# Optimization experiments

Measured on AMD Instinct MI355X. Metric: run time of the kernel, lower is better.

Reference implementation:

```python
import jax, jax.numpy as jnp
import numpy as np

SEG = 8  # conv1d groups


def _grouped_mix(y, W2, b2, seg):
    # y: [b, C_in, L]; W2: [C_out, C_in//seg]; grouped 1x1 conv1d
    b_, cin, L = y.shape
    cout = W2.shape[0]
    yg = y.reshape(b_, seg, cin // seg, L)
    Wg = W2.reshape(seg, cout // seg, cin // seg)
    z = jnp.einsum('bgcl,goc->bgol', yg, Wg).reshape(b_, cout, L)
    return z + b2[None, :, None]


def _mix_h(x, W1, b1, W2, b2):
    # x: [b,h,w,d]
    b_, H, Wd, D = x.shape
    y = jnp.einsum('bhwd,ed->bhwe', x, W1) + b1            # 1x1 conv2d -> [b,h,w,e]
    y = jnp.transpose(y, (0, 3, 1, 2)).reshape(b_, -1, Wd)  # 'b d h w -> b (d h) w'
    z = _grouped_mix(y, W2, b2, SEG)                        # [b, h*h, w]
    attn = jax.nn.softmax(
        z.reshape(b_, H, H, Wd).transpose(0, 3, 1, 2), axis=-1)  # [b,w,h1,h2]
    xr = jnp.transpose(x, (0, 2, 1, 3))                     # [b,w,h,d]
    out = jnp.einsum('bwij,bwjd->bwid', attn, xr)
    return jnp.transpose(out, (0, 2, 1, 3))                 # [b,h,w,d]


def _mix_w(x, W1, b1, W2, b2):
    # x: [b,h,w,d]
    b_, H, Wd, D = x.shape
    y = jnp.einsum('bhwd,ed->bhwe', x, W1) + b1             # [b,h,w,e]
    y = jnp.transpose(y, (0, 3, 2, 1)).reshape(b_, -1, H)   # 'b d w h -> b (d w) h'
    z = _grouped_mix(y, W2, b2, SEG)                        # [b, w*w, h]
    attn = jax.nn.softmax(
        z.reshape(b_, Wd, Wd, H).transpose(0, 3, 1, 2), axis=-1)  # [b,h,w1,w2]
    return jnp.einsum('bhij,bhjd->bhid', attn, x)           # [b,h,w,d]


def setup_inputs() -> dict:
    key = jax.random.key(0)
    ks = jax.random.split(key, 16)
    B, H, W, D, E = 64, 32, 32, 384, 2
    s = 0.05
    return {
        'x':   jax.random.normal(ks[0], (B, H, W, D), jnp.float32),
        'Wc':  jax.random.normal(ks[1], (D, D), jnp.float32) * s,
        'bc':  jnp.zeros((D,), jnp.float32),
        'Wo':  jax.random.normal(ks[2], (D, D), jnp.float32) * s,
        'bo':  jnp.zeros((D,), jnp.float32),
        'W1h': jax.random.normal(ks[3], (E, D), jnp.float32) * s,
        'b1h': jnp.zeros((E,), jnp.float32),
        'W2h': jax.random.normal(ks[4], (H * H, E * H // SEG), jnp.float32) * s,
        'b2h': jnp.zeros((H * H,), jnp.float32),
        'W1w': jax.random.normal(ks[5], (E, D), jnp.float32) * s,
        'b1w': jnp.zeros((E,), jnp.float32),
        'W2w': jax.random.normal(ks[6], (W * W, E * W // SEG), jnp.float32) * s,
        'b2w': jnp.zeros((W * W,), jnp.float32),
    }


def reference(x, Wc, bc, Wo, bo, W1h, b1h, W2h, b2h, W1w, b1w, W2w, b2w):
    Y_c = jnp.einsum('bhwd,od->bhwo', x, Wc) + bc
    Y_h = _mix_h(x, W1h, b1h, W2h, b2h)
    Y_w = _mix_w(x, W1w, b1w, W2w, b2w)
    Y = Y_h + Y_w + Y_c
    return jnp.einsum('bhwd,od->bhwo', Y, Wo) + bo
```

## Files before the change

### kernel.cpp

```cpp
#include <hip/hip_runtime.h>
#include <hip/hip_bf16.h>
#include <cstdint>
#include <cstddef>

typedef __bf16 bf16;
typedef __attribute__((ext_vector_type(8))) __bf16 bf16x8;
typedef __attribute__((ext_vector_type(4))) float floatx4;

#define NPIX 65536

__device__ inline void async_copy16(void* lds, const void* g) {
    __builtin_amdgcn_global_load_lds(
        (const __attribute__((address_space(1))) void*)g,
        (__attribute__((address_space(3))) void*)lds, 16, 0, 0);
}

__global__ void k_prep_w(const float* __restrict__ Wc, const float* __restrict__ bc,
                         const float* __restrict__ Wo, const float* __restrict__ bo,
                         bf16* __restrict__ Wfull, float* __restrict__ bco) {
    int blk = blockIdx.x;
    int t = threadIdx.x;
    if (blk < 384) {
        int o = blk;
        float acc = 0.f;
        for (int d = 0; d < 384; ++d)
            acc += Wo[o * 384 + d] * Wc[d * 384 + t];
        Wfull[(size_t)o * 768 + t]       = (bf16)Wo[o * 384 + t];
        Wfull[(size_t)o * 768 + 384 + t] = (bf16)acc;
    } else {
        int o = t;
        float acc = bo[o];
        for (int d = 0; d < 384; ++d)
            acc += Wo[o * 384 + d] * bc[d];
        bco[o] = acc;
    }
}

__global__ void k_proj(const float* __restrict__ xf, bf16* __restrict__ xb,
                       const float* __restrict__ W1h, const float* __restrict__ b1h,
                       const float* __restrict__ W1w, const float* __restrict__ b1w,
                       float* __restrict__ yh, float* __restrict__ yw) {
    int t  = threadIdx.x;
    int lg = t & 7;
    int pg = t >> 3;
    int p  = blockIdx.x * 32 + pg;
    int b = p >> 10, h = (p >> 5) & 31, w = p & 31;
    const float4* xp4 = (const float4*)(xf + (size_t)p * 384);
    float a0 = 0.f, a1 = 0.f, a2 = 0.f, a3 = 0.f;
#pragma unroll
    for (int j = 0; j < 6; ++j) {
        int c = j * 8 + lg;
        float4 xa = xp4[c * 2], xcv = xp4[c * 2 + 1];
        bf16x8 v;
        v[0] = (bf16)xa.x; v[1] = (bf16)xa.y; v[2] = (bf16)xa.z; v[3] = (bf16)xa.w;
        v[4] = (bf16)xcv.x; v[5] = (bf16)xcv.y; v[6] = (bf16)xcv.z; v[7] = (bf16)xcv.w;
        *(bf16x8*)(xb + ((size_t)(c >> 1) * NPIX + p) * 16 + (c & 1) * 8) = v;
        const float4* h0 = (const float4*)(W1h + c * 8);
        const float4* h1 = (const float4*)(W1h + 384 + c * 8);
        const float4* w0 = (const float4*)(W1w + c * 8);
        const float4* w1 = (const float4*)(W1w + 384 + c * 8);
        float4 h0a = h0[0], h0b = h0[1], h1a = h1[0], h1b = h1[1];
        float4 w0a = w0[0], w0b = w0[1], w1a = w1[0], w1b = w1[1];
        a0 += xa.x*h0a.x + xa.y*h0a.y + xa.z*h0a.z + xa.w*h0a.w
            + xcv.x*h0b.x + xcv.y*h0b.y + xcv.z*h0b.z + xcv.w*h0b.w;
        a1 += xa.x*h1a.x + xa.y*h1a.y + xa.z*h1a.z + xa.w*h1a.w
            + xcv.x*h1b.x + xcv.y*h1b.y + xcv.z*h1b.z + xcv.w*h1b.w;
        a2 += xa.x*w0a.x + xa.y*w0a.y + xa.z*w0a.z + xa.w*w0a.w
            + xcv.x*w0b.x + xcv.y*w0b.y + xcv.z*w0b.z + xcv.w*w0b.w;
        a3 += xa.x*w1a.x + xa.y*w1a.y + xa.z*w1a.z + xa.w*w1a.w
            + xcv.x*w1b.x + xcv.y*w1b.y + xcv.z*w1b.z + xcv.w*w1b.w;
    }
#pragma unroll
    for (int m = 1; m < 8; m <<= 1) {
        a0 += __shfl_xor(a0, m, 64);
        a1 += __shfl_xor(a1, m, 64);
        a2 += __shfl_xor(a2, m, 64);
        a3 += __shfl_xor(a3, m, 64);
    }
    if (lg == 0) {
        yh[((b * 2 + 0) * 32 + h) * 32 + w] = a0 + b1h[0];
        yh[((b * 2 + 1) * 32 + h) * 32 + w] = a1 + b1h[1];
        yw[((b * 2 + 0) * 32 + w) * 32 + h] = a2 + b1w[0];
        yw[((b * 2 + 1) * 32 + w) * 32 + h] = a3 + b1w[1];
    }
}

__global__ void k_attn(const float* __restrict__ yproj,
                       const float* __restrict__ W2, const float* __restrict__ b2,
                       bf16* __restrict__ attn) {
    int blk = blockIdx.x;
    int bi = blk >> 5, r1 = blk & 31;
    int g = r1 >> 2;
    int cb = g * 8;
    int e = cb >> 5, rb = cb & 31;
    int lane = threadIdx.x;
    int l = lane & 31, half = lane >> 5;
    float yv[8];
    const float* ybase = yproj + (((bi * 2 + e) * 32 + rb) * 32 + l);
#pragma unroll
    for (int c = 0; c < 8; ++c) yv[c] = ybase[c * 32];
    float z[16];
#pragma unroll
    for (int jj = 0; jj < 16; ++jj) {
        int r2 = half * 16 + jj;
        int row = r1 * 32 + r2;
        const float4* wp = (const float4*)(W2 + (size_t)row * 8);
        float4 wa = wp[0], wb = wp[1];
        z[jj] = b2[row]
              + yv[0]*wa.x + yv[1]*wa.y + yv[2]*wa.z + yv[3]*wa.w
              + yv[4]*wb.x + yv[5]*wb.y + yv[6]*wb.z + yv[7]*wb.w;
    }
    float m = -1e30f;
#pragma unroll
    for (int jj = 0; jj < 16; ++jj) m = fmaxf(m, z[jj]);
    m = fmaxf(m, __shfl_xor(m, 32, 64));
    float s = 0.f;
#pragma unroll
    for (int jj = 0; jj < 16; ++jj) { z[jj] = __expf(z[jj] - m); s += z[jj]; }
    s += __shfl_xor(s, 32, 64);
    float inv = 1.f / s;
    bf16x8 o0, o1;
#pragma unroll
    for (int jj = 0; jj < 8; ++jj) o0[jj] = (bf16)(z[jj] * inv);
#pragma unroll
    for (int jj = 0; jj < 8; ++jj) o1[jj] = (bf16)(z[8 + jj] * inv);
    bf16x8* dst = (bf16x8*)(attn + ((((size_t)bi * 32 + l) * 32 + r1) * 32 + half * 16));
    dst[0] = o0;
    dst[1] = o1;
}

__global__ __launch_bounds__(256) void k_mix(const bf16* __restrict__ x,
                                             const bf16* __restrict__ attn_h,
                                             const bf16* __restrict__ attn_w,
                                             bf16* __restrict__ T) {
    __shared__ bf16 Xs[1024 * 16];
    __shared__ bf16 Ts[1024 * 16];
    int n = blockIdx.x;
    int idx = n >> 3;
    int bi = (n & 7) * 8 + idx / 24;
    int c  = idx % 24;
    int tid = threadIdx.x;
    int wv = tid >> 6, lane = tid & 63;
    int n16 = lane & 15, quad = lane >> 4;

    const bf16* src = x + ((size_t)c * NPIX + bi * 1024) * 16;
#pragma unroll
    for (int it = 0; it < 8; ++it)
        async_copy16((char*)Xs + (it * 256 + tid) * 16,
                     (const char*)src + (size_t)(it * 256 + tid) * 16);
    __syncthreads();

#pragma unroll
    for (int wl = 0; wl < 8; ++wl) {
        int w = wv * 8 + wl;
        const bf16* ab = attn_h + ((size_t)(bi * 32 + w) * 32) * 32;
        bf16x8 af0 = *(const bf16x8*)(ab + n16 * 32 + quad * 8);
        bf16x8 af1 = *(const bf16x8*)(ab + (16 + n16) * 32 + quad * 8);
        bf16x8 bfrag;
#pragma unroll
        for (int i = 0; i < 8; ++i) {
            int j = quad * 8 + i;
            bfrag[i] = Xs[(j * 32 + w) * 16 + n16];
        }
        floatx4 c0 = {0.f, 0.f, 0.f, 0.f}, c1 = {0.f, 0.f, 0.f, 0.f};
        c0 = __builtin_amdgcn_mfma_f32_16x16x32_bf16(af0, bfrag, c0, 0, 0, 0);
        c1 = __builtin_amdgcn_mfma_f32_16x16x32_bf16(af1, bfrag, c1, 0, 0, 0);
#pragma unroll
        for (int rr = 0; rr < 4; ++rr) {
            int h0 = quad * 4 + rr;
            Ts[(h0 * 32 + w) * 16 + n16]        = (bf16)c0[rr];
            Ts[((16 + h0) * 32 + w) * 16 + n16] = (bf16)c1[rr];
        }
    }
    __syncthreads();

#pragma unroll
    for (int hl = 0; hl < 8; ++hl) {
        int h = wv * 8 + hl;
        const bf16* ab = attn_w + ((size_t)(bi * 32 + h) * 32) * 32;
        bf16x8 af0 = *(const bf16x8*)(ab + n16 * 32 + quad * 8);
        bf16x8 af1 = *(const bf16x8*)(ab + (16 + n16) * 32 + quad * 8);
        bf16x8 bfrag;
#pragma unroll
        for (int i = 0; i < 8; ++i) {
            int j = quad * 8 + i;
            bfrag[i] = Xs[(h * 32 + j) * 16 + n16];
        }
        floatx4 c0 = {0.f, 0.f, 0.f, 0.f}, c1 = {0.f, 0.f, 0.f, 0.f};
        c0 = __builtin_amdgcn_mfma_f32_16x16x32_bf16(af0, bfrag, c0, 0, 0, 0);
        c1 = __builtin_amdgcn_mfma_f32_16x16x32_bf16(af1, bfrag, c1, 0, 0, 0);
#pragma unroll
        for (int rr = 0; rr < 4; ++rr) {
            int w0 = quad * 4 + rr;
            Xs[(h * 32 + w0) * 16 + n16] =
                (bf16)(c0[rr] + (float)Ts[(h * 32 + w0) * 16 + n16]);
            Xs[(h * 32 + 16 + w0) * 16 + n16] =
                (bf16)(c1[rr] + (float)Ts[(h * 32 + 16 + w0) * 16 + n16]);
        }
    }
    __syncthreads();

    bf16* dst = T + ((size_t)c * NPIX + bi * 1024) * 16;
#pragma unroll
    for (int it = 0; it < 8; ++it)
        *(bf16x8*)(dst + (size_t)(it * 256 + tid) * 8) =
            *(const bf16x8*)(Xs + (it * 256 + tid) * 8);
}

__global__ __launch_bounds__(256) void k_gemm(const bf16* __restrict__ T, const bf16* __restrict__ x,
                                              const bf16* __restrict__ Wfull, const float* __restrict__ bco,
                                              float* __restrict__ out) {
    __shared__ bf16 As[2][128 * 64];
    __shared__ bf16 Bs[2][128 * 64];
    int bx = blockIdx.x;
    int gid = (bx & 7) * 192 + (bx >> 3);
    int nt = gid % 3, pt = gid / 3;
    int obase = nt * 128;
    int pbase = pt * 128;
    int tid = threadIdx.x;
    int wv = tid >> 6, lane = tid & 63;
    int wm = wv & 1, wn = wv >> 1;
    int n16 = lane & 15, quad = lane >> 4;
    int srow = lane >> 3, sch = lane & 7;
    floatx4 zero = {0.f, 0.f, 0.f, 0.f};
    floatx4 acc[4][4];
#pragma unroll
    for (int i = 0; i < 4; ++i)
#pragma unroll
        for (int j = 0; j < 4; ++j) acc[i][j] = zero;

    const bf16* Bg0 = Wfull + (size_t)obase * 768;

    auto stage = [&](int buf, int kt) {
        const bf16* Ag = (kt < 6) ? T : x;
        size_t arow = ((size_t)(((kt < 6) ? kt : kt - 6) * 4 + (sch >> 1))) * NPIX + pbase;
#pragma unroll
        for (int it = 0; it < 4; ++it) {
            int r0 = wv * 32 + it * 8;
            async_copy16((void*)(As[buf] + r0 * 64 + lane * 8),
                         (const void*)(Ag + (arow + r0 + srow) * 16 + (sch & 1) * 8));
            async_copy16((void*)(Bs[buf] + r0 * 64 + lane * 8),
                         (const void*)(Bg0 + (size_t)(r0 + srow) * 768 + kt * 64 + sch * 8));
        }
    };

    stage(0, 0);
    __syncthreads();
    int buf = 0;
    for (int kt = 0; kt < 12; ++kt) {
        if (kt < 11) stage(buf ^ 1, kt + 1);
#pragma unroll
        for (int ks = 0; ks < 2; ++ks) {
            bf16x8 a[4], b[4];
#pragma unroll
            for (int i = 0; i < 4; ++i)
                a[i] = *(const bf16x8*)(As[buf] + (wm * 64 + i * 16 + n16) * 64 + ks * 32 + quad * 8);
#pragma unroll
            for (int j = 0; j < 4; ++j)
                b[j] = *(const bf16x8*)(Bs[buf] + (wn * 64 + j * 16 + n16) * 64 + ks * 32 + quad * 8);
#pragma unroll
            for (int i = 0; i < 4; ++i)
#pragma unroll
                for (int j = 0; j < 4; ++j)
                    acc[i][j] = __builtin_amdgcn_mfma_f32_16x16x32_bf16(a[i], b[j], acc[i][j], 0, 0, 0);
        }
        __syncthreads();
        buf ^= 1;
    }
#pragma unroll
    for (int j = 0; j < 4; ++j) {
        int o = obase + wn * 64 + j * 16 + n16;
        float bcv = bco[o];
#pragma unroll
        for (int i = 0; i < 4; ++i) {
            int prow = pbase + wm * 64 + i * 16 + quad * 4;
#pragma unroll
            for (int r = 0; r < 4; ++r)
                out[(size_t)(prow + r) * 384 + o] = acc[i][j][r] + bcv;
        }
    }
}

extern "C" void kernel_launch(void* const* d_in, const int* in_sizes, int n_in,
                              void* d_out, int out_size, void* d_ws, size_t ws_size,
                              hipStream_t stream) {
    const float* x   = (const float*)d_in[0];
    const float* Wc  = (const float*)d_in[1];
    const float* bc  = (const float*)d_in[2];
    const float* Wo  = (const float*)d_in[3];
    const float* bo  = (const float*)d_in[4];
    const float* W1h = (const float*)d_in[5];
    const float* b1h = (const float*)d_in[6];
    const float* W2h = (const float*)d_in[7];
    const float* b2h = (const float*)d_in[8];
    const float* W1w = (const float*)d_in[9];
    const float* b1w = (const float*)d_in[10];
    const float* W2w = (const float*)d_in[11];
    const float* b2w = (const float*)d_in[12];
    float* out = (float*)d_out;

    char* ws = (char*)d_ws;
    size_t off = 0;
    auto alloc = [&](size_t bytes) {
        void* p = ws + off;
        off = (off + bytes + 255) & ~(size_t)255;
        return p;
    };
    bf16*  xb     = (bf16*)alloc((size_t)NPIX * 384 * 2);
    float* yh     = (float*)alloc((size_t)131072 * 4);
    float* yw     = (float*)alloc((size_t)131072 * 4);
    bf16*  attn_h = (bf16*)alloc((size_t)2097152 * 2);
    bf16*  attn_w = (bf16*)alloc((size_t)2097152 * 2);
    bf16*  T      = (bf16*)alloc((size_t)NPIX * 384 * 2);
    bf16*  Wfull  = (bf16*)alloc((size_t)384 * 768 * 2);
    float* bco    = (float*)alloc((size_t)384 * 4);

    hipLaunchKernelGGL(k_prep_w, dim3(385), dim3(384), 0, stream, Wc, bc, Wo, bo, Wfull, bco);
    hipLaunchKernelGGL(k_proj, dim3(2048), dim3(256), 0, stream, x, xb, W1h, b1h, W1w, b1w, yh, yw);
    hipLaunchKernelGGL(k_attn, dim3(2048), dim3(64), 0, stream, yh, W2h, b2h, attn_h);
    hipLaunchKernelGGL(k_attn, dim3(2048), dim3(64), 0, stream, yw, W2w, b2w, attn_w);
    hipLaunchKernelGGL(k_mix, dim3(1536), dim3(256), 0, stream, xb, attn_h, attn_w, T);
    hipLaunchKernelGGL(k_gemm, dim3(1536), dim3(256), 0, stream, T, xb, Wfull, bco, out);
}
```

Measured before the change: 341.6 us.

## Swizzle GEMM LDS tiles, merge attn launches, and block weight-prep rows

The GEMM's LDS tiles get an XOR swizzle: the column chunk each lane fetches is XORed with its row index, and reads use the matching swizzled offset. This is meant to remove bank conflicts on the 16-byte fragment reads. The two k_attn launches become a single launch of 4096 blocks that picks the h or w inputs by block index, saving one kernel launch. k_prep_w now has each block compute 8 output rows, so each Wc load is reused 8 times, which cuts the grid from 385 blocks to 49 at the cost of lower parallelism in that kernel.

```diff
diff --git a/kernel.cpp b/kernel.cpp
--- a/kernel.cpp
+++ b/kernel.cpp
@@ -20,13 +20,20 @@
                          bf16* __restrict__ Wfull, float* __restrict__ bco) {
     int blk = blockIdx.x;
     int t = threadIdx.x;
-    if (blk < 384) {
-        int o = blk;
-        float acc = 0.f;
-        for (int d = 0; d < 384; ++d)
-            acc += Wo[o * 384 + d] * Wc[d * 384 + t];
-        Wfull[(size_t)o * 768 + t]       = (bf16)Wo[o * 384 + t];
-        Wfull[(size_t)o * 768 + 384 + t] = (bf16)acc;
+    if (blk < 48) {
+        int o0 = blk * 8;
+        float acc[8] = {0.f, 0.f, 0.f, 0.f, 0.f, 0.f, 0.f, 0.f};
+        for (int d = 0; d < 384; ++d) {
+            float wc = Wc[d * 384 + t];
+#pragma unroll
+            for (int r = 0; r < 8; ++r)
+                acc[r] += Wo[(o0 + r) * 384 + d] * wc;
+        }
+#pragma unroll
+        for (int r = 0; r < 8; ++r) {
+            Wfull[(size_t)(o0 + r) * 768 + t]       = (bf16)Wo[(o0 + r) * 384 + t];
+            Wfull[(size_t)(o0 + r) * 768 + 384 + t] = (bf16)acc[r];
+        }
     } else {
         int o = t;
         float acc = bo[o];
@@ -85,10 +92,14 @@
     }
 }
 
-__global__ void k_attn(const float* __restrict__ yproj,
-                       const float* __restrict__ W2, const float* __restrict__ b2,
-                       bf16* __restrict__ attn) {
+__global__ void k_attn(const float* __restrict__ yh_in, const float* __restrict__ yw_in,
+                       const float* __restrict__ W2h, const float* __restrict__ b2h,
+                       const float* __restrict__ W2w, const float* __restrict__ b2w,
+                       bf16* __restrict__ attn_h, bf16* __restrict__ attn_w) {
     int blk = blockIdx.x;
+    const float* yproj; const float* W2; const float* b2; bf16* attn;
+    if (blk < 2048) { yproj = yh_in; W2 = W2h; b2 = b2h; attn = attn_h; }
+    else            { yproj = yw_in; W2 = W2w; b2 = b2w; attn = attn_w; blk -= 2048; }
     int bi = blk >> 5, r1 = blk & 31;
     int g = r1 >> 2;
     int cb = g * 8;
@@ -222,6 +233,7 @@
     int wm = wv & 1, wn = wv >> 1;
     int n16 = lane & 15, quad = lane >> 4;
     int srow = lane >> 3, sch = lane & 7;
+    int scha = sch ^ srow;
     floatx4 zero = {0.f, 0.f, 0.f, 0.f};
     floatx4 acc[4][4];
 #pragma unroll
@@ -233,31 +245,34 @@
 
     auto stage = [&](int buf, int kt) {
         const bf16* Ag = (kt < 6) ? T : x;
-        size_t arow = ((size_t)(((kt < 6) ? kt : kt - 6) * 4 + (sch >> 1))) * NPIX + pbase;
+        int k6 = (kt < 6) ? kt : kt - 6;
+        size_t arow = ((size_t)(k6 * 4 + (scha >> 1))) * NPIX + pbase;
 #pragma unroll
         for (int it = 0; it < 4; ++it) {
             int r0 = wv * 32 + it * 8;
             async_copy16((void*)(As[buf] + r0 * 64 + lane * 8),
-                         (const void*)(Ag + (arow + r0 + srow) * 16 + (sch & 1) * 8));
+                         (const void*)(Ag + (arow + r0 + srow) * 16 + (scha & 1) * 8));
             async_copy16((void*)(Bs[buf] + r0 * 64 + lane * 8),
-                         (const void*)(Bg0 + (size_t)(r0 + srow) * 768 + kt * 64 + sch * 8));
+                         (const void*)(Bg0 + (size_t)(r0 + srow) * 768 + kt * 64 + scha * 8));
         }
     };
 
     stage(0, 0);
     __syncthreads();
     int buf = 0;
+    int sa = n16 & 7;
     for (int kt = 0; kt < 12; ++kt) {
         if (kt < 11) stage(buf ^ 1, kt + 1);
 #pragma unroll
         for (int ks = 0; ks < 2; ++ks) {
+            int coff = ((ks * 4 + quad) ^ sa) * 8;
             bf16x8 a[4], b[4];
 #pragma unroll
             for (int i = 0; i < 4; ++i)
-                a[i] = *(const bf16x8*)(As[buf] + (wm * 64 + i * 16 + n16) * 64 + ks * 32 + quad * 8);
+                a[i] = *(const bf16x8*)(As[buf] + (wm * 64 + i * 16 + n16) * 64 + coff);
 #pragma unroll
             for (int j = 0; j < 4; ++j)
-                b[j] = *(const bf16x8*)(Bs[buf] + (wn * 64 + j * 16 + n16) * 64 + ks * 32 + quad * 8);
+                b[j] = *(const bf16x8*)(Bs[buf] + (wn * 64 + j * 16 + n16) * 64 + coff);
 #pragma unroll
             for (int i = 0; i < 4; ++i)
 #pragma unroll
@@ -315,10 +330,9 @@
     bf16*  Wfull  = (bf16*)alloc((size_t)384 * 768 * 2);
     float* bco    = (float*)alloc((size_t)384 * 4);
 
-    hipLaunchKernelGGL(k_prep_w, dim3(385), dim3(384), 0, stream, Wc, bc, Wo, bo, Wfull, bco);
+    hipLaunchKernelGGL(k_prep_w, dim3(49), dim3(384), 0, stream, Wc, bc, Wo, bo, Wfull, bco);
     hipLaunchKernelGGL(k_proj, dim3(2048), dim3(256), 0, stream, x, xb, W1h, b1h, W1w, b1w, yh, yw);
-    hipLaunchKernelGGL(k_attn, dim3(2048), dim3(64), 0, stream, yh, W2h, b2h, attn_h);
-    hipLaunchKernelGGL(k_attn, dim3(2048), dim3(64), 0, stream, yw, W2w, b2w, attn_w);
+    hipLaunchKernelGGL(k_attn, dim3(4096), dim3(64), 0, stream, yh, yw, W2h, b2h, W2w, b2w, attn_h, attn_w);
     hipLaunchKernelGGL(k_mix, dim3(1536), dim3(256), 0, stream, xb, attn_h, attn_w, T);
     hipLaunchKernelGGL(k_gemm, dim3(1536), dim3(256), 0, stream, T, xb, Wfull, bco, out);
 }
```

After: 354.0 us. 1.04x slower.
